# Kernel optimization log

Hardware: AMD Instinct MI355X
Metric: run time of the kernel (lower is better)

The kernel has to match this reference:

```python
import jax, jax.numpy as jnp
import numpy as np

D = 1024
H = 16
T_BLOCK = 2048


def setup_inputs() -> dict:
    key = jax.random.key(0)
    ks = jax.random.split(key, 12)
    B, T = 2, 2048
    s = lambda k, shape: jax.random.normal(k, shape, jnp.float32) * 0.02
    return {
        "x": jax.random.normal(ks[0], (B, T, D), jnp.float32),
        # layernorms
        "ln1_g": jnp.ones((D,), jnp.float32), "ln1_b": jnp.zeros((D,), jnp.float32),
        "ln2_g": jnp.ones((D,), jnp.float32), "ln2_b": jnp.zeros((D,), jnp.float32),
        # attention qkv projection ([in,out] layout) and output proj
        "w_qkv": s(ks[1], (D, 3 * D)), "b_qkv": jnp.zeros((3 * D,), jnp.float32),
        "w_o": s(ks[2], (D, D)), "b_o": jnp.zeros((D,), jnp.float32),
        # MLP
        "w_fc1": s(ks[3], (D, 4 * D)), "b_fc1": jnp.zeros((4 * D,), jnp.float32),
        "w_fc2": s(ks[4], (4 * D, D)), "b_fc2": jnp.zeros((D,), jnp.float32),
    }


def _layernorm(x, g, b, eps=1e-5):
    mu = jnp.mean(x, axis=-1, keepdims=True)
    var = jnp.var(x, axis=-1, keepdims=True)
    return (x - mu) * jax.lax.rsqrt(var + eps) * g + b


def _attention(x, w_qkv, b_qkv, w_o, b_o):
    B, T, C = x.shape
    hd = C // H
    qkv = x @ w_qkv + b_qkv                      # [B,T,3C]
    q, k, v = jnp.split(qkv, 3, axis=-1)
    split = lambda t: t.reshape(B, T, H, hd).transpose(0, 2, 1, 3)  # [B,H,T,hd]
    q, k, v = split(q), split(k), split(v)
    att = jnp.einsum("bhqd,bhkd->bhqk", q, k) / jnp.sqrt(jnp.float32(hd))
    causal = jnp.tril(jnp.ones((T, T), bool))
    att = jnp.where(causal[None, None], att, -jnp.inf)
    att = jax.nn.softmax(att, axis=-1)
    y = jnp.einsum("bhqk,bhkd->bhqd", att, v)    # [B,H,T,hd]
    y = y.transpose(0, 2, 1, 3).reshape(B, T, C)
    return y @ w_o + b_o


def reference(x, ln1_g, ln1_b, ln2_g, ln2_b, w_qkv, b_qkv, w_o, b_o,
              w_fc1, b_fc1, w_fc2, b_fc2):
    # dropout is identity in eval mode
    x = x + _attention(_layernorm(x, ln1_g, ln1_b), w_qkv, b_qkv, w_o, b_o)
    h = jax.nn.gelu(_layernorm(x, ln2_g, ln2_b) @ w_fc1 + b_fc1)
    return x + (h @ w_fc2 + b_fc2)
```

## Files before the change

### kernel.cpp

```cpp
#include <hip/hip_runtime.h>
#include <hip/hip_bf16.h>


using bf16 = __bf16;
using bf16x8 = __attribute__((ext_vector_type(8))) __bf16;
using floatx4 = __attribute__((ext_vector_type(4))) float;

#define D_ 1024
#define T_ 2048
#define B_ 2
#define H_ 16

static __device__ __forceinline__ bf16 f2bf(float f) { return (bf16)f; }

static __device__ __forceinline__ void async16(const void* g, void* l) {
  __builtin_amdgcn_global_load_lds(
      (const __attribute__((address_space(1))) void*)g,
      (__attribute__((address_space(3))) void*)l, 16, 0, 0);
}

static __device__ __forceinline__ float gelu_f(float v) {
  const float u2 = 1.5957691216057308f * (v + 0.044715f * v * v * v);
  return v / (1.0f + __expf(-u2));
}

static __device__ __forceinline__ void ln_row(const float* __restrict__ x,
                                              const float* __restrict__ g,
                                              const float* __restrict__ bsh,
                                              bf16* __restrict__ out,
                                              int row, int tid, float* red) {
  const float4 v = ((const float4*)(x + (size_t)row * D_))[tid];
  float s = v.x + v.y + v.z + v.w;
  float s2 = v.x * v.x + v.y * v.y + v.z * v.z + v.w * v.w;
  for (int off = 32; off; off >>= 1) {
    s += __shfl_xor(s, off);
    s2 += __shfl_xor(s2, off);
  }
  const int wave = tid >> 6, lane = tid & 63;
  if (lane == 0) { red[wave] = s; red[wave + 4] = s2; }
  __syncthreads();
  s = red[0] + red[1] + red[2] + red[3];
  s2 = red[4] + red[5] + red[6] + red[7];
  const float mu = s * (1.0f / D_);
  const float rstd = rsqrtf(s2 * (1.0f / D_) - mu * mu + 1e-5f);
  const float4 gv = ((const float4*)g)[tid];
  const float4 bv = ((const float4*)bsh)[tid];
  bf16 o[4] __attribute__((aligned(8)));
  o[0] = f2bf((v.x - mu) * rstd * gv.x + bv.x);
  o[1] = f2bf((v.y - mu) * rstd * gv.y + bv.y);
  o[2] = f2bf((v.z - mu) * rstd * gv.z + bv.z);
  o[3] = f2bf((v.w - mu) * rstd * gv.w + bv.w);
  *(ushort4*)(out + (size_t)row * D_ + tid * 4) = *(const ushort4*)o;
}

__global__ void transpose_cast_all(const float* __restrict__ w_qkv,
                                   const float* __restrict__ w_o,
                                   const float* __restrict__ w_fc1,
                                   const float* __restrict__ w_fc2,
                                   bf16* __restrict__ wqkvT, bf16* __restrict__ woT,
                                   bf16* __restrict__ wfc1T, bf16* __restrict__ wfc2T,
                                   const float* __restrict__ x,
                                   const float* __restrict__ ln1_g,
                                   const float* __restrict__ ln1_b,
                                   bf16* __restrict__ ln1) {
  int t = blockIdx.x;
  __shared__ float tile[32][33];
  if (t >= 12288) {
    const int tid = threadIdx.y * 32 + threadIdx.x;
    ln_row(x, ln1_g, ln1_b, ln1, t - 12288, tid, &tile[0][0]);
    return;
  }
  const float* in;
  bf16* out;
  int K, N, nx;
  if (t < 3072)      { in = w_qkv; out = wqkvT; K = 1024; N = 3072; nx = 96;  }
  else if (t < 4096) { in = w_o;   out = woT;   K = 1024; N = 1024; nx = 32;  t -= 3072; }
  else if (t < 8192) { in = w_fc1; out = wfc1T; K = 1024; N = 4096; nx = 128; t -= 4096; }
  else               { in = w_fc2; out = wfc2T; K = 4096; N = 1024; nx = 32;  t -= 8192; }
  const int n0 = (t % nx) * 32, k0 = (t / nx) * 32;
  const int tx = threadIdx.x, ty = threadIdx.y;
  for (int i = 0; i < 32; i += 8)
    tile[ty + i][tx] = in[(size_t)(k0 + ty + i) * N + n0 + tx];
  __syncthreads();
  for (int i = 0; i < 32; i += 8)
    out[(size_t)(n0 + ty + i) * K + k0 + tx] = f2bf(tile[tx][ty + i]);
}

__global__ __launch_bounds__(256)
void ln_kernel(const float* __restrict__ x, const float* __restrict__ g,
               const float* __restrict__ bsh, bf16* __restrict__ out) {
  __shared__ float red[8];
  ln_row(x, g, bsh, out, blockIdx.x, threadIdx.x, red);
}

template <int EPI>
__global__ __launch_bounds__(256)
void gemm_bt_sb(const bf16* __restrict__ A, const bf16* __restrict__ Bt,
                const float* __restrict__ bias, const float* __restrict__ res,
                void* __restrict__ Cout, int M, int N, int K) {
  __shared__ __align__(16) bf16 As[128][64];
  __shared__ __align__(16) bf16 Bs[128][64];
  const int tid = threadIdx.x;
  const int wave = tid >> 6, lane = tid & 63;
  const int quad = lane >> 4, l16 = lane & 15;
  const int wr = wave >> 1, wc = wave & 1;
  const int bm = blockIdx.x * 128, bn = blockIdx.y * 128;
  const int lrow8 = lane >> 3;
  const int lcol = (((lane & 7) ^ lrow8) * 8);

  floatx4 acc[4][4] = {};

  for (int k0 = 0; k0 < K; k0 += 64) {
    __syncthreads();
    for (int c = 0; c < 4; c++) {
      const int r = wave * 32 + c * 8;
      async16(&A[(size_t)(bm + r + lrow8) * K + k0 + lcol], &As[r][0]);
      async16(&Bt[(size_t)(bn + r + lrow8) * K + k0 + lcol], &Bs[r][0]);
    }
    __syncthreads();
    for (int ks = 0; ks < 2; ks++) {
      const int fc = ((quad + ks * 4) ^ (l16 & 7)) * 8;
      bf16x8 af[4], bfr[4];
      for (int mt = 0; mt < 4; mt++)
        af[mt] = *(const bf16x8*)&As[wr * 64 + mt * 16 + l16][fc];
      for (int nt = 0; nt < 4; nt++)
        bfr[nt] = *(const bf16x8*)&Bs[wc * 64 + nt * 16 + l16][fc];
      for (int mt = 0; mt < 4; mt++)
        for (int nt = 0; nt < 4; nt++)
          acc[mt][nt] = __builtin_amdgcn_mfma_f32_16x16x32_bf16(
              af[mt], bfr[nt], acc[mt][nt], 0, 0, 0);
    }
  }

  for (int mt = 0; mt < 4; mt++) {
    for (int nt = 0; nt < 4; nt++) {
      const int col = bn + wc * 64 + nt * 16 + l16;
      const float bcol = bias[col];
      for (int i = 0; i < 4; i++) {
        const int row = bm + wr * 64 + mt * 16 + quad * 4 + i;
        float v = acc[mt][nt][i] + bcol;
        if (EPI == 0) {
          ((bf16*)Cout)[(size_t)row * N + col] = f2bf(v);
        } else if (EPI == 1) {
          ((bf16*)Cout)[(size_t)row * N + col] = f2bf(gelu_f(v));
        } else {
          ((float*)Cout)[(size_t)row * N + col] = v + res[(size_t)row * N + col];
        }
      }
    }
  }
}

template <int EPI>
__global__ __launch_bounds__(256)
void gemm_bt(const bf16* __restrict__ A, const bf16* __restrict__ Bt,
             const float* __restrict__ bias, const float* __restrict__ res,
             void* __restrict__ Cout, int M, int N, int K) {
  __shared__ __align__(16) bf16 As[2][128][64];
  __shared__ __align__(16) bf16 Bs[2][128][64];
  const int tid = threadIdx.x;
  const int wave = tid >> 6, lane = tid & 63;
  const int quad = lane >> 4, l16 = lane & 15;
  const int wr = wave >> 1, wc = wave & 1;
  const int bm = blockIdx.x * 128, bn = blockIdx.y * 128;
  const int lrow8 = lane >> 3;
  const int lcol = (((lane & 7) ^ lrow8) * 8);

  const bf16* aBase = &A[(size_t)(bm + wave * 32 + lrow8) * K + lcol];
  const bf16* bBase = &Bt[(size_t)(bn + wave * 32 + lrow8) * K + lcol];

  auto stage = [&](int buf, int kk) {
    const int k0 = kk * 64;
    for (int c = 0; c < 4; c++) {
      async16(aBase + (size_t)c * 8 * K + k0, &As[buf][wave * 32 + c * 8][0]);
      async16(bBase + (size_t)c * 8 * K + k0, &Bs[buf][wave * 32 + c * 8][0]);
    }
  };

  floatx4 acc[4][4] = {};
  const int nsteps = K >> 6;

  stage(0, 0);
  if (nsteps > 1) stage(1, 1);
  int cur = 0;
  for (int t = 0; t < nsteps; ++t) {
    if (t < nsteps - 1)
      asm volatile("s_waitcnt vmcnt(8)" ::: "memory");
    else
      asm volatile("s_waitcnt vmcnt(0)" ::: "memory");
    __builtin_amdgcn_s_barrier();
    __builtin_amdgcn_sched_barrier(0);
    for (int ks = 0; ks < 2; ks++) {
      const int fc = ((quad + ks * 4) ^ (l16 & 7)) * 8;
      bf16x8 af[4], bfr[4];
      for (int mt = 0; mt < 4; mt++)
        af[mt] = *(const bf16x8*)&As[cur][wr * 64 + mt * 16 + l16][fc];
      for (int nn = 0; nn < 4; nn++)
        bfr[nn] = *(const bf16x8*)&Bs[cur][wc * 64 + nn * 16 + l16][fc];
      for (int mt = 0; mt < 4; mt++)
        for (int nn = 0; nn < 4; nn++)
          acc[mt][nn] = __builtin_amdgcn_mfma_f32_16x16x32_bf16(
              af[mt], bfr[nn], acc[mt][nn], 0, 0, 0);
    }
    __builtin_amdgcn_sched_barrier(0);
    __builtin_amdgcn_s_barrier();
    if (t + 2 < nsteps) stage(cur, t + 2);
    cur ^= 1;
  }

  for (int mt = 0; mt < 4; mt++) {
    for (int nn = 0; nn < 4; nn++) {
      const int col = bn + wc * 64 + nn * 16 + l16;
      const float bcol = bias[col];
      for (int i = 0; i < 4; i++) {
        const int row = bm + wr * 64 + mt * 16 + quad * 4 + i;
        float v = acc[mt][nn][i] + bcol;
        if (EPI == 0) {
          ((bf16*)Cout)[(size_t)row * N + col] = f2bf(v);
        } else if (EPI == 1) {
          ((bf16*)Cout)[(size_t)row * N + col] = f2bf(gelu_f(v));
        } else {
          ((float*)Cout)[(size_t)row * N + col] = v + res[(size_t)row * N + col];
        }
      }
    }
  }
}

template <int EPI>
__global__ __launch_bounds__(256)
void gemm64_k128(const bf16* __restrict__ A, const bf16* __restrict__ Bt,
                 const float* __restrict__ bias, const float* __restrict__ res,
                 void* __restrict__ Cout, int M, int N, int K) {
  __shared__ __align__(16) bf16 As[64][128];
  __shared__ __align__(16) bf16 Bs[128][128];
  const int tid = threadIdx.x;
  const int wave = tid >> 6, lane = tid & 63;
  const int quad = lane >> 4, l16 = lane & 15;
  const int wr = wave >> 1, wc = wave & 1;
  const int bm = blockIdx.x * 64, bn = blockIdx.y * 128;
  const int sr = lane >> 4;
  const int pchunk = lane & 15;

  floatx4 acc[2][4] = {};

  for (int k0 = 0; k0 < K; k0 += 128) {
    __syncthreads();
    for (int c = 0; c < 4; c++) {
      const int base = wave * 16 + c * 4;
      const int scol = (pchunk ^ ((c * 4 + sr) & 15)) * 8;
      async16(&A[(size_t)(bm + base + sr) * K + k0 + scol], &As[base][0]);
    }
    for (int c = 0; c < 8; c++) {
      const int base = wave * 32 + c * 4;
      const int scol = (pchunk ^ ((c * 4 + sr) & 15)) * 8;
      async16(&Bt[(size_t)(bn + base + sr) * K + k0 + scol], &Bs[base][0]);
    }
    __syncthreads();
    for (int ks = 0; ks < 4; ks++) {
      const int fc = ((quad + ks * 4) ^ l16) * 8;
      bf16x8 af[2], bfr[4];
      for (int mt = 0; mt < 2; mt++)
        af[mt] = *(const bf16x8*)&As[wr * 32 + mt * 16 + l16][fc];
      for (int nt = 0; nt < 4; nt++)
        bfr[nt] = *(const bf16x8*)&Bs[wc * 64 + nt * 16 + l16][fc];
      for (int mt = 0; mt < 2; mt++)
        for (int nt = 0; nt < 4; nt++)
          acc[mt][nt] = __builtin_amdgcn_mfma_f32_16x16x32_bf16(
              af[mt], bfr[nt], acc[mt][nt], 0, 0, 0);
    }
  }

  for (int mt = 0; mt < 2; mt++) {
    for (int nt = 0; nt < 4; nt++) {
      const int col = bn + wc * 64 + nt * 16 + l16;
      const float bcol = bias[col];
      for (int i = 0; i < 4; i++) {
        const int row = bm + wr * 32 + mt * 16 + quad * 4 + i;
        float v = acc[mt][nt][i] + bcol;
        if (EPI == 0) {
          ((bf16*)Cout)[(size_t)row * N + col] = f2bf(v);
        } else if (EPI == 1) {
          ((bf16*)Cout)[(size_t)row * N + col] = f2bf(gelu_f(v));
        } else {
          ((float*)Cout)[(size_t)row * N + col] = v + res[(size_t)row * N + col];
        }
      }
    }
  }
}

__global__ __launch_bounds__(512)
void attn_kernel(const bf16* __restrict__ qkv, bf16* __restrict__ y) {
  const int bh = blockIdx.y, b = bh >> 4, h = bh & 15;
  const int tile = (blockIdx.y & 16) ? (int)blockIdx.x : (15 - (int)blockIdx.x);
  const int q0 = tile * 128;
  const int tid = threadIdx.x, wave = tid >> 6, lane = tid & 63;
  const int quad = lane >> 4, l16 = lane & 15;
  const int l7 = l16 & 7;
  const int w16 = wave * 16;

  __shared__ __align__(16) bf16 Ks[2][64][64];
  __shared__ __align__(16) bf16 Vts[2][64][64];
  __shared__ __align__(16) bf16 Ps[128][64];

  const size_t bbase = (size_t)b * T_ * 3072 + (size_t)h * 64;
  const bf16* Qg = qkv + bbase;
  const bf16* Kg = qkv + bbase + 1024;
  const bf16* Vg = qkv + bbase + 2048;

  bf16x8 ones;
  for (int j = 0; j < 8; j++) ones[j] = f2bf(1.0f);

  const int kr = tid >> 3, kch = tid & 7;
  const int kcol = ((kch ^ (kr & 7)) * 8);
  const int vk = tid & 63, vd = tid >> 6;

  bf16x8 qf[2];
  for (int ks = 0; ks < 2; ks++) {
    bf16x8 t = *(const bf16x8*)
        &Qg[(size_t)(q0 + w16 + l16) * 3072 + ks * 32 + quad * 8];
    for (int j = 0; j < 8; j++) t[j] = f2bf((float)t[j] * 0.125f);
    qf[ks] = t;
  }

  int4 kreg = *(const int4*)&Kg[(size_t)kr * 3072 + kch * 8];
  bf16x8 vreg = *(const bf16x8*)&Vg[(size_t)vk * 3072 + vd * 8];
  *(int4*)&Ks[0][kr][kcol] = kreg;
  for (int j = 0; j < 8; j++)
    Vts[0][vd * 8 + j][((vk >> 3) ^ j) * 8 + (vk & 7)] = vreg[j];

  floatx4 accY[4] = {};
  floatx4 accL = {};

  const int kend = q0 + 64;
  int bc = 0;
  for (int kc = 0; kc <= kend; kc += 64, bc ^= 1) {
    __syncthreads();

    const bool pf = (kc < kend);
    if (pf) {
      kreg = *(const int4*)&Kg[(size_t)(kc + 64 + kr) * 3072 + kch * 8];
      vreg = *(const bf16x8*)&Vg[(size_t)(kc + 64 + vk) * 3072 + vd * 8];
    }

    floatx4 s[4];
    for (int nt = 0; nt < 4; nt++) {
      const bf16* krow = &Ks[bc][nt * 16 + l16][0];
      bf16x8 kf0 = *(const bf16x8*)&krow[(quad ^ l7) * 8];
      bf16x8 kf1 = *(const bf16x8*)&krow[((4 + quad) ^ l7) * 8];
      floatx4 t = {};
      t = __builtin_amdgcn_mfma_f32_16x16x32_bf16(qf[0], kf0, t, 0, 0, 0);
      t = __builtin_amdgcn_mfma_f32_16x16x32_bf16(qf[1], kf1, t, 0, 0, 0);
      s[nt] = t;
    }
    if (kc + 64 > q0 + w16) {
      for (int nt = 0; nt < 4; nt++)
        for (int i = 0; i < 4; i++) {
          const int c = kc + nt * 16 + l16;
          const int r = q0 + w16 + quad * 4 + i;
          if (c > r) s[nt][i] = -1e30f;
        }
    }

    for (int i = 0; i < 4; i++) {
      const int pr = quad * 4 + i;
      bf16* prow = &Ps[w16 + pr][0];
      for (int nt = 0; nt < 4; nt++)
        prow[(((nt * 2 + (l16 >> 3)) ^ (pr & 7)) * 8) + l7] =
            f2bf(__expf(s[nt][i] - 8.0f));
    }
    __builtin_amdgcn_wave_barrier();

    for (int ks = 0; ks < 2; ks++) {
      bf16x8 pa = *(const bf16x8*)&Ps[w16 + l16][((ks * 4 + quad) ^ l7) * 8];
      for (int dt = 0; dt < 4; dt++) {
        bf16x8 vb =
            *(const bf16x8*)&Vts[bc][dt * 16 + l16][((ks * 4 + quad) ^ l7) * 8];
        accY[dt] =
            __builtin_amdgcn_mfma_f32_16x16x32_bf16(pa, vb, accY[dt], 0, 0, 0);
      }
      accL = __builtin_amdgcn_mfma_f32_16x16x32_bf16(pa, ones, accL, 0, 0, 0);
    }

    if (pf) {
      *(int4*)&Ks[bc ^ 1][kr][kcol] = kreg;
      for (int j = 0; j < 8; j++)
        Vts[bc ^ 1][vd * 8 + j][((vk >> 3) ^ j) * 8 + (vk & 7)] = vreg[j];
    }
  }

  for (int i = 0; i < 4; i++) {
    const float linv = 1.0f / accL[i];
    const int r = q0 + w16 + quad * 4 + i;
    for (int dt = 0; dt < 4; dt++)
      y[(size_t)(b * T_ + r) * D_ + h * 64 + dt * 16 + l16] =
          f2bf(accY[dt][i] * linv);
  }
}

extern "C" void kernel_launch(void* const* d_in, const int* in_sizes, int n_in,
                              void* d_out, int out_size, void* d_ws, size_t ws_size,
                              hipStream_t stream) {
  const float* x     = (const float*)d_in[0];
  const float* ln1_g = (const float*)d_in[1];
  const float* ln1_b = (const float*)d_in[2];
  const float* ln2_g = (const float*)d_in[3];
  const float* ln2_b = (const float*)d_in[4];
  const float* w_qkv = (const float*)d_in[5];
  const float* b_qkv = (const float*)d_in[6];
  const float* w_o   = (const float*)d_in[7];
  const float* b_o   = (const float*)d_in[8];
  const float* w_fc1 = (const float*)d_in[9];
  const float* b_fc1 = (const float*)d_in[10];
  const float* w_fc2 = (const float*)d_in[11];
  const float* b_fc2 = (const float*)d_in[12];

  char* p = (char*)d_ws;
  bf16* wqkvT = (bf16*)p; p += (size_t)3072 * 1024 * 2;
  bf16* woT   = (bf16*)p; p += (size_t)1024 * 1024 * 2;
  bf16* wfc1T = (bf16*)p; p += (size_t)4096 * 1024 * 2;
  bf16* wfc2T = (bf16*)p; p += (size_t)1024 * 4096 * 2;
  bf16* ln1   = (bf16*)p; p += (size_t)4096 * 1024 * 2;
  bf16* qkv   = (bf16*)p; p += (size_t)4096 * 3072 * 2;
  bf16* yb    = (bf16*)p; p += (size_t)4096 * 1024 * 2;
  float* x2   = (float*)p; p += (size_t)4096 * 1024 * 4;
  bf16* ln2   = (bf16*)p; p += (size_t)4096 * 1024 * 2;
  bf16* hb    = (bf16*)p; p += (size_t)4096 * 4096 * 2;

  transpose_cast_all<<<dim3(16384), dim3(32, 8), 0, stream>>>(
      w_qkv, w_o, w_fc1, w_fc2, wqkvT, woT, wfc1T, wfc2T,
      x, ln1_g, ln1_b, ln1);

  gemm_bt_sb<0><<<dim3(32, 24), 256, 0, stream>>>(ln1, wqkvT, b_qkv, nullptr, qkv,
                                                  4096, 3072, 1024);
  attn_kernel<<<dim3(16, 32), 512, 0, stream>>>(qkv, yb);
  gemm64_k128<2><<<dim3(64, 8), 256, 0, stream>>>(yb, woT, b_o, x, x2,
                                                  4096, 1024, 1024);
  ln_kernel<<<4096, 256, 0, stream>>>(x2, ln2_g, ln2_b, ln2);
  gemm_bt<1><<<dim3(32, 32), 256, 0, stream>>>(ln2, wfc1T, b_fc1, nullptr, hb,
                                               4096, 4096, 1024);
  gemm64_k128<2><<<dim3(64, 8), 256, 0, stream>>>(hb, wfc2T, b_fc2, x2, (float*)d_out,
                                                  4096, 1024, 4096);
}
```

Before: 303.6 us.

## Add 256x256-tile double-buffered GEMM with 8 waves for FC1

Adds a new GEMM kernel that computes a 256x256 output tile per 512-thread block. It double-buffers K=64 slabs loaded with async global-to-LDS copies, uses XOR-swizzled LDS, interleaves barriers with MFMA clusters, and raises wave priority during MFMA. The FC1+GELU GEMM now uses it with a 16x16 grid instead of the 128x128-tile kernel, aiming for more operand reuse per LDS load and overlap of loads with compute. The trade-off is fewer blocks (256 on a GPU with many CUs), higher register pressure from 32 accumulators per thread, and 128KB of LDS per block.

```diff
diff --git a/kernel.cpp b/kernel.cpp
--- a/kernel.cpp
+++ b/kernel.cpp
@@ -138,6 +138,99 @@
       const float bcol = bias[col];
       for (int i = 0; i < 4; i++) {
         const int row = bm + wr * 64 + mt * 16 + quad * 4 + i;
+        float v = acc[mt][nt][i] + bcol;
+        if (EPI == 0) {
+          ((bf16*)Cout)[(size_t)row * N + col] = f2bf(v);
+        } else if (EPI == 1) {
+          ((bf16*)Cout)[(size_t)row * N + col] = f2bf(gelu_f(v));
+        } else {
+          ((float*)Cout)[(size_t)row * N + col] = v + res[(size_t)row * N + col];
+        }
+      }
+    }
+  }
+}
+
+template <int EPI>
+__global__ __launch_bounds__(512, 2)
+void gemm256p4(const bf16* __restrict__ A, const bf16* __restrict__ Bt,
+               const float* __restrict__ bias, const float* __restrict__ res,
+               void* __restrict__ Cout, int M, int N, int K) {
+  __shared__ __align__(16) bf16 As[2][256][64];
+  __shared__ __align__(16) bf16 Bs[2][256][64];
+  const int tid = threadIdx.x;
+  const int wave = tid >> 6, lane = tid & 63;
+  const int quad = lane >> 4, l16 = lane & 15;
+  const int wr = wave >> 2, wc = wave & 3;
+  const int bm = blockIdx.x * 256, bn = blockIdx.y * 256;
+  const int lrow8 = lane >> 3;
+  const int lcol = (((lane & 7) ^ lrow8) * 8);
+
+  const bf16* aBase = &A[(size_t)(bm + wave * 32 + lrow8) * K + lcol];
+  const bf16* bBase = &Bt[(size_t)(bn + wave * 32 + lrow8) * K + lcol];
+
+  auto stage = [&](int buf, int kk) {
+    const int k0 = kk * 64;
+#pragma unroll
+    for (int c = 0; c < 4; c++) {
+      async16(aBase + (size_t)c * 8 * K + k0, &As[buf][wave * 32 + c * 8][0]);
+      async16(bBase + (size_t)c * 8 * K + k0, &Bs[buf][wave * 32 + c * 8][0]);
+    }
+  };
+
+  floatx4 acc[8][4] = {};
+  const int nsteps = K >> 6;
+
+  stage(0, 0);
+  if (nsteps > 1) stage(1, 1);
+  int cur = 0;
+  for (int t = 0; t < nsteps; ++t) {
+    if (t < nsteps - 1)
+      asm volatile("s_waitcnt vmcnt(8)" ::: "memory");
+    else
+      asm volatile("s_waitcnt vmcnt(0)" ::: "memory");
+    __builtin_amdgcn_s_barrier();
+    __builtin_amdgcn_sched_barrier(0);
+#pragma unroll
+    for (int ks = 0; ks < 2; ks++) {
+      const int fc = ((quad + ks * 4) ^ (l16 & 7)) * 8;
+#pragma unroll
+      for (int half = 0; half < 2; half++) {
+        bf16x8 af[4], bfr[4];
+#pragma unroll
+        for (int m = 0; m < 4; m++)
+          af[m] = *(const bf16x8*)
+              &As[cur][wr * 128 + (half * 4 + m) * 16 + l16][fc];
+#pragma unroll
+        for (int nt = 0; nt < 4; nt++)
+          bfr[nt] = *(const bf16x8*)&Bs[cur][wc * 64 + nt * 16 + l16][fc];
+        __builtin_amdgcn_s_barrier();
+        __builtin_amdgcn_sched_barrier(0);
+        __builtin_amdgcn_s_setprio(1);
+#pragma unroll
+        for (int m = 0; m < 4; m++)
+#pragma unroll
+          for (int nt = 0; nt < 4; nt++)
+            acc[half * 4 + m][nt] = __builtin_amdgcn_mfma_f32_16x16x32_bf16(
+                af[m], bfr[nt], acc[half * 4 + m][nt], 0, 0, 0);
+        __builtin_amdgcn_s_setprio(0);
+        __builtin_amdgcn_sched_barrier(0);
+      }
+    }
+    __builtin_amdgcn_s_barrier();
+    if (t + 2 < nsteps) stage(cur, t + 2);
+    cur ^= 1;
+  }
+
+#pragma unroll
+  for (int mt = 0; mt < 8; mt++) {
+#pragma unroll
+    for (int nt = 0; nt < 4; nt++) {
+      const int col = bn + wc * 64 + nt * 16 + l16;
+      const float bcol = bias[col];
+#pragma unroll
+      for (int i = 0; i < 4; i++) {
+        const int row = bm + wr * 128 + mt * 16 + quad * 4 + i;
         float v = acc[mt][nt][i] + bcol;
         if (EPI == 0) {
           ((bf16*)Cout)[(size_t)row * N + col] = f2bf(v);
@@ -438,8 +531,8 @@
   gemm64_k128<2><<<dim3(64, 8), 256, 0, stream>>>(yb, woT, b_o, x, x2,
                                                   4096, 1024, 1024);
   ln_kernel<<<4096, 256, 0, stream>>>(x2, ln2_g, ln2_b, ln2);
-  gemm_bt<1><<<dim3(32, 32), 256, 0, stream>>>(ln2, wfc1T, b_fc1, nullptr, hb,
-                                               4096, 4096, 1024);
+  gemm256p4<1><<<dim3(16, 16), 512, 0, stream>>>(ln2, wfc1T, b_fc1, nullptr, hb,
+                                                 4096, 4096, 1024);
   gemm64_k128<2><<<dim3(64, 8), 256, 0, stream>>>(hb, wfc2T, b_fc2, x2, (float*)d_out,
                                                   4096, 1024, 4096);
 }
```

New measurement: 312.6 us. 1.03x slower.
